# Kernel tuning notes

Hardware: AMD Instinct MI355X
Metric: run time of the kernel (lower is better)

Reference implementation:

```python
import jax, jax.numpy as jnp
import numpy as np

N_NODES = 50000
N_EDGES = 200000
D_IN = 128
D = 256
N_LAYERS = 4
N_REL = 4
NUM_M = 1024
NUM_R = 64
DIM_Y = 2
LAM_VI = 0.1
LAM_REG = 0.1
TEMP = 0.3  # RelaxedBernoulli temperature used by FNP sample_bipartite
EPS = 1e-8


def _glorot(key, shape):
    fan_in = shape[-2] if len(shape) >= 2 else shape[0]
    return (jax.random.normal(key, shape, dtype=jnp.float32) / np.float32(np.sqrt(fan_in)))


def setup_inputs() -> dict:
    key = jax.random.key(0)
    ks = jax.random.split(key, 16)
    x = jax.random.normal(ks[0], (N_NODES, D_IN), jnp.float32)
    edge_index = jax.random.randint(ks[1], (2, N_EDGES), 0, N_NODES)
    edge_type = jax.random.randint(ks[2], (N_EDGES,), 0, N_REL)
    batch = jnp.sort(jax.random.randint(ks[3], (N_NODES,), 0, NUM_M))
    yM = jax.random.randint(ks[4], (NUM_M,), 0, DIM_Y)
    yR = jax.random.randint(ks[5], (NUM_R,), 0, DIM_Y)
    H_R = jax.random.normal(ks[6], (NUM_R, D), jnp.float32)
    node_W = _glorot(ks[7], (D_IN, D)); node_b = jnp.zeros((D,), jnp.float32)
    gcn_Wr = _glorot(ks[8], (N_LAYERS, N_REL, D, D))
    gcn_Wroot = _glorot(ks[9], (N_LAYERS, D, D))
    gcn_b = jnp.zeros((N_LAYERS, D), jnp.float32)
    pg_logscale = jnp.array([0.5 * np.log(D)], jnp.float32)  # log(sqrt(dim_u)) init
    pu_W = _glorot(ks[10], (D, 2 * D)); pu_b = jnp.zeros((2 * D,), jnp.float32)
    qz_W = _glorot(ks[11], (D, 2 * D)); qz_b = jnp.zeros((2 * D,), jnp.float32)
    out_W1 = _glorot(ks[12], (2 * D, 256)); out_b1 = jnp.zeros((256,), jnp.float32)
    out_W2 = _glorot(ks[13], (256, DIM_Y)); out_b2 = jnp.zeros((DIM_Y,), jnp.float32)
    return dict(x=x, edge_index=edge_index, edge_type=edge_type, batch=batch, yM=yM, yR=yR,
                H_R=H_R, node_W=node_W, node_b=node_b, gcn_Wr=gcn_Wr, gcn_Wroot=gcn_Wroot,
                gcn_b=gcn_b, pg_logscale=pg_logscale, pu_W=pu_W, pu_b=pu_b, qz_W=qz_W,
                qz_b=qz_b, out_W1=out_W1, out_b1=out_b1, out_W2=out_W2, out_b2=out_b2)


def _cond_trans(x, edge_index, edge_type, batch, node_W, node_b, gcn_Wr, gcn_Wroot, gcn_b):
    # AtomEncoder replaced by Linear (num_relations==1 branch); then 4 RGCNConv layers
    n = x.shape[0]
    src, dst = edge_index[0], edge_index[1]
    feats = x @ node_W + node_b
    for l in range(N_LAYERS):
        # per-relation transform of all nodes: [N_REL, N, D]
        h_rel = jnp.einsum('nd,rdh->rnh', feats, gcn_Wr[l])
        msg = h_rel[edge_type, src]  # gather per-edge messages [E, D]
        comp = edge_type * n + dst   # (relation, dst) composite segment id
        cnt = jax.ops.segment_sum(jnp.ones((msg.shape[0],), feats.dtype), comp,
                                  num_segments=N_REL * n)
        msg = msg / jnp.clip(cnt[comp], 1.0)[:, None]  # mean aggregation per relation
        agg = jax.ops.segment_sum(msg, dst, num_segments=n)
        feats = agg + feats @ gcn_Wroot[l] + gcn_b[l]
        if l < N_LAYERS - 1:
            feats = jax.nn.relu(feats)
    gsum = jax.ops.segment_sum(feats, batch, num_segments=NUM_M)
    gcnt = jax.ops.segment_sum(jnp.ones((n,), feats.dtype), batch, num_segments=NUM_M)
    return gsum / jnp.clip(gcnt, 1.0)[:, None]  # global_mean_pool


def _normal_logprob(v, mean, logscale):
    return -0.5 * np.float32(np.log(2 * np.pi)) - logscale - 0.5 * ((v - mean) * jnp.exp(-logscale)) ** 2


def _logitexp(logp):
    # logit of exp(logp): logp - log(1 - exp(logp))
    return logp - jnp.log(jnp.clip(-jnp.expm1(logp), 1e-20))


def reference(x, edge_index, edge_type, batch, yM, yR, H_R, node_W, node_b, gcn_Wr,
              gcn_Wroot, gcn_b, pg_logscale, pu_W, pu_b, qz_W, qz_b, out_W1, out_b1,
              out_W2, out_b2):
    H_M = _cond_trans(x, edge_index, edge_type, batch, node_W, node_b, gcn_Wr, gcn_Wroot, gcn_b)
    H_all = jnp.concatenate([H_R, H_M], axis=0)
    key = jax.random.key(42)
    k_u, k_a, k_zm, k_zr = jax.random.split(key, 4)

    # p_u: ReLU -> Linear -> split mean / logscale; reparameterized sample
    pu = jax.nn.relu(H_all) @ pu_W + pu_b
    pu_mean, pu_ls = pu[:, :D], pu[:, D:]
    u = pu_mean + jnp.exp(pu_ls) * jax.random.normal(k_u, pu_mean.shape, pu_mean.dtype)
    u_R, u_M = u[:NUM_R], u[NUM_R:]

    # sample_bipartite(u_M, u_R, pairwise_g): relaxed Bernoulli over pairwise logits
    d2 = jnp.sum((u_M[:, None, :] - u_R[None, :, :]) ** 2, axis=-1)  # [M, R]
    logits_A = _logitexp(-0.5 * d2 / jnp.exp(pg_logscale[0]))
    U = jax.random.uniform(k_a, logits_A.shape, minval=1e-6, maxval=1.0 - 1e-6)
    A = jax.nn.sigmoid((logits_A + jnp.log(U) - jnp.log1p(-U)) / TEMP)
    An = A / (jnp.sum(A, axis=1, keepdims=True) + EPS)  # norm_graph

    # q_z head
    qz = jax.nn.relu(H_all) @ qz_W + qz_b
    qz_mean, qz_ls = qz[:, :D], qz[:, D:]
    z_M = qz_mean[NUM_R:] + jnp.exp(qz_ls[NUM_R:]) * jax.random.normal(k_zm, (NUM_M, D), qz_mean.dtype)
    pz_mean_M = An @ qz_mean[:NUM_R]
    pz_ls_M = An @ qz_ls[:NUM_R]
    log_pqz_M = jnp.sum(_normal_logprob(z_M, pz_mean_M, pz_ls_M)
                        - _normal_logprob(z_M, qz_mean[NUM_R:], qz_ls[NUM_R:]))
    z_R = qz_mean[:NUM_R] + jnp.exp(qz_ls[:NUM_R]) * jax.random.normal(k_zr, (NUM_R, D), qz_mean.dtype)

    # prediction head (use_plus=True -> concat z and u)
    rep_M = jnp.concatenate([z_M, u_M], axis=1)
    logits_M = jax.nn.relu(rep_M @ out_W1 + out_b1) @ out_W2 + out_b2
    log_pyM = jnp.take_along_axis(jax.nn.log_softmax(logits_M, axis=-1), yM[:, None], axis=1)[:, 0]
    prediction_loss = -(jnp.sum(log_pyM) + LAM_VI * log_pqz_M) / np.float32(NUM_M)

    rep_R = jnp.concatenate([z_R, u_R], axis=1)
    logits_R = jax.nn.relu(rep_R @ out_W1 + out_b1) @ out_W2 + out_b2
    rationale_loss = -jnp.mean(jnp.take_along_axis(jax.nn.log_softmax(logits_R, axis=-1), yR[:, None], axis=1)[:, 0])

    # mode 'E' distance regularizer
    pd = jnp.sqrt(jnp.clip(jnp.sum((u_R[:, None, :] - u_M[None, :, :]) ** 2, axis=-1), 1e-12))  # [R, M]
    idx = jnp.arange(NUM_R // 2)[:, None] + (1 - yM)[None, :] * (NUM_R // 2)
    reg = jnp.mean(jnp.take_along_axis(pd, idx, axis=0))

    return prediction_loss + rationale_loss - LAM_REG * reg
```

## Files before the change

### kernel.cpp

```cpp
#include <hip/hip_runtime.h>
#include <stdint.h>

#define N_NODESC 50000
#define N_EDGESC 200000
#define D_INC 128
#define DC 256
#define N_LAYERSC 4
#define N_RELC 4
#define NUM_MC 1024
#define NUM_RC 64
#define NBLK_SCAN ((N_NODESC + 255) / 256)

typedef __attribute__((ext_vector_type(4))) float floatx4;
typedef __attribute__((ext_vector_type(8))) short short8;

__host__ __device__ __forceinline__ uint32_t rotl32(uint32_t x, int r){ return (x<<r)|(x>>(32-r)); }

__host__ __device__ inline void tf2x32(uint32_t k0, uint32_t k1, uint32_t x0, uint32_t x1,
                                       uint32_t* o0, uint32_t* o1){
  uint32_t k2 = k0 ^ k1 ^ 0x1BD11BDAu;
#define TFR(r) { x0 += x1; x1 = rotl32(x1, (r)); x1 ^= x0; }
  x0 += k0; x1 += k1;
  TFR(13) TFR(15) TFR(26) TFR(6)
  x0 += k1; x1 += k2 + 1u;
  TFR(17) TFR(29) TFR(16) TFR(24)
  x0 += k2; x1 += k0 + 2u;
  TFR(13) TFR(15) TFR(26) TFR(6)
  x0 += k0; x1 += k1 + 3u;
  TFR(17) TFR(29) TFR(16) TFR(24)
  x0 += k1; x1 += k2 + 4u;
  TFR(13) TFR(15) TFR(26) TFR(6)
  x0 += k2; x1 += k0 + 5u;
#undef TFR
  *o0 = x0; *o1 = x1;
}

__device__ __forceinline__ float erfinv_f32(float x){
  float w = -log1pf(-x*x);
  float p;
  if (w < 5.0f){
    w -= 2.5f;
    p = 2.81022636e-08f;
    p = fmaf(p, w, 3.43273939e-07f);
    p = fmaf(p, w, -3.5233877e-06f);
    p = fmaf(p, w, -4.39150654e-06f);
    p = fmaf(p, w, 0.00021858087f);
    p = fmaf(p, w, -0.00125372503f);
    p = fmaf(p, w, -0.00417768164f);
    p = fmaf(p, w, 0.246640727f);
    p = fmaf(p, w, 1.50140941f);
  } else {
    w = sqrtf(w) - 3.0f;
    p = -0.000200214257f;
    p = fmaf(p, w, 0.000100950558f);
    p = fmaf(p, w, 0.00134934322f);
    p = fmaf(p, w, -0.00367342844f);
    p = fmaf(p, w, 0.00573950773f);
    p = fmaf(p, w, -0.0076224613f);
    p = fmaf(p, w, 0.00943887047f);
    p = fmaf(p, w, 1.00167406f);
    p = fmaf(p, w, 2.83297682f);
  }
  return p*x;
}

__device__ __forceinline__ float bits_to_unit(uint32_t b){
  return __uint_as_float((b >> 9) | 0x3f800000u) - 1.0f;
}

__device__ __forceinline__ float bits_to_normal(uint32_t b){
  float f = bits_to_unit(b);
  const float lo = -0.99999994f;
  float u = f * (1.0f - lo) + lo;
  u = fmaxf(u, lo);
  return 1.41421356f * erfinv_f32(u);
}

__device__ __forceinline__ float waveReduce(float v){
  #pragma unroll
  for (int m = 1; m < 64; m <<= 1) v += __shfl_xor(v, m, 64);
  return v;
}

__device__ __forceinline__ ushort f2bf(float f){
  uint32_t u = __float_as_uint(f);
  uint32_t r = u + 0x7fffu + ((u>>16)&1u);
  return (ushort)(r>>16);
}
__device__ __forceinline__ float bf2f(ushort h){
  return __uint_as_float(((uint32_t)h)<<16);
}

typedef const __attribute__((address_space(1))) void* gas_t;
typedef __attribute__((address_space(3))) void* las_t;
__device__ __forceinline__ void gld16(const void* g, void* l){
  __builtin_amdgcn_global_load_lds((gas_t)g, (las_t)l, 16, 0, 0);
}

__global__ __launch_bounds__(256) void k_zero4(float4* p, int n4){
  int i = blockIdx.x*256 + threadIdx.x;
  if (i < n4) p[i] = make_float4(0.f,0.f,0.f,0.f);
}

__global__ __launch_bounds__(256) void k_count(const int* __restrict__ ei, const int* __restrict__ et,
                                               float* __restrict__ cnt, int* __restrict__ deg){
  int e = blockIdx.x*256 + threadIdx.x;
  if (e >= N_EDGESC) return;
  int r = et[e], dstv = ei[N_EDGESC + e];
  atomicAdd(&cnt[(size_t)r*N_NODESC + dstv], 1.0f);
  atomicAdd(&deg[dstv], 1);
}

__global__ __launch_bounds__(256) void k_scan1(const int* __restrict__ deg, int* __restrict__ bsum){
  int i = blockIdx.x*256 + threadIdx.x;
  int v = (i < N_NODESC) ? deg[i] : 0;
  #pragma unroll
  for (int m = 1; m < 64; m <<= 1) v += __shfl_xor(v, m, 64);
  __shared__ int ws_[4];
  if ((threadIdx.x & 63) == 0) ws_[threadIdx.x >> 6] = v;
  __syncthreads();
  if (threadIdx.x == 0) bsum[blockIdx.x] = ws_[0]+ws_[1]+ws_[2]+ws_[3];
}

__global__ __launch_bounds__(256) void k_scan2(int* __restrict__ bsum, int* __restrict__ boff){
  __shared__ int s[256];
  int t = threadIdx.x;
  s[t] = (t < NBLK_SCAN) ? bsum[t] : 0;
  __syncthreads();
  if (t == 0){
    int run = 0;
    for (int i = 0; i < NBLK_SCAN; i++){ int v = s[i]; s[i] = run; run += v; }
  }
  __syncthreads();
  if (t < NBLK_SCAN) boff[t] = s[t];
}

__global__ __launch_bounds__(256) void k_scan3(const int* __restrict__ deg, const int* __restrict__ boff,
                                               int* __restrict__ rowptr){
  int i = blockIdx.x*256 + threadIdx.x;
  int lane = threadIdx.x & 63, w = threadIdx.x >> 6;
  int d = (i < N_NODESC) ? deg[i] : 0;
  int v = d;
  #pragma unroll
  for (int off = 1; off < 64; off <<= 1){
    int t = __shfl_up(v, off, 64);
    if (lane >= off) v += t;
  }
  __shared__ int wt[4];
  if (lane == 63) wt[w] = v;
  __syncthreads();
  int wo = 0;
  for (int k = 0; k < w; k++) wo += wt[k];
  int ex = boff[blockIdx.x] + wo + v - d;
  if (i <= N_NODESC) rowptr[i] = ex;
}

__global__ __launch_bounds__(256) void k_fill2(const int* __restrict__ ei, const int* __restrict__ et,
                                               const float* __restrict__ cnt, const int* __restrict__ rowptr,
                                               int* __restrict__ cursor, int* __restrict__ ep,
                                               float* __restrict__ einvc){
  int e = blockIdx.x*256 + threadIdx.x;
  if (e >= N_EDGESC) return;
  int src = ei[e], dstv = ei[N_EDGESC + e], r = et[e];
  int pos = rowptr[dstv] + atomicAdd(&cursor[dstv], 1);
  ep[pos] = src | (r << 16);
  einvc[pos] = 1.0f / fmaxf(cnt[(size_t)r*N_NODESC + dstv], 1.0f);
}

__global__ __launch_bounds__(256) void k_bnd(const int* __restrict__ batch, int* __restrict__ grow){
  int i = blockIdx.x*256 + threadIdx.x;
  if (i >= N_NODESC) return;
  int b = batch[i];
  if (i == 0){ for (int g = 0; g <= b; g++) grow[g] = 0; }
  else {
    int pb = batch[i-1];
    for (int g = pb+1; g <= b; g++) grow[g] = i;
  }
  if (i == N_NODESC-1){ for (int g = b+1; g <= NUM_MC; g++) grow[g] = N_NODESC; }
}

__global__ __launch_bounds__(256) void k_wt(const float* __restrict__ src, ushort* __restrict__ dst,
                                            int K, int N, int total){
  int idx = blockIdx.x*256 + threadIdx.x;
  if (idx >= total) return;
  int k = idx / N, n = idx - k*N;
  dst[(size_t)n*K + k] = f2bf(src[idx]);
}

__global__ __launch_bounds__(256) void k_wcat(const float* __restrict__ Wroot, const float* __restrict__ Wr,
                                              ushort* __restrict__ Wcat){
  int idx = blockIdx.x*256 + threadIdx.x;
  if (idx >= N_LAYERSC*1280*DC) return;
  int l = idx / (1280*DC), rem = idx - l*(1280*DC);
  int n = rem / DC, k = rem - n*DC;
  float v;
  if (n < DC) v = Wroot[((size_t)l*DC + k)*DC + n];
  else {
    int r = (n - DC) >> 8, nn = (n - DC) & 255;
    v = Wr[(((size_t)l*N_RELC + r)*DC + k)*DC + nn];
  }
  Wcat[idx] = f2bf(v);
}

__global__ __launch_bounds__(256) void k_cvt4(const float4* __restrict__ src, ushort4* __restrict__ dst,
                                              int n4){
  int i = blockIdx.x*256 + threadIdx.x;
  if (i >= n4) return;
  float4 v = src[i];
  ushort4 o; o.x=f2bf(v.x); o.y=f2bf(v.y); o.z=f2bf(v.z); o.w=f2bf(v.w);
  dst[i] = o;
}

__global__ __launch_bounds__(256) void k_gather(const ushort* __restrict__ slabs, const float* __restrict__ bias,
                                                ushort* __restrict__ curbOut, int relu,
                                                const int* __restrict__ rowptr, const int* __restrict__ ep,
                                                const float* __restrict__ einvc){
  int dstv = blockIdx.x*4 + (threadIdx.x >> 6);
  if (dstv >= N_NODESC) return;
  int lane = threadIdx.x & 63;
  int beg = rowptr[dstv], end = rowptr[dstv+1];
  const ushort4 w0 = *(const ushort4*)(slabs + (size_t)dstv*DC + lane*4);
  const float4 bv = *(const float4*)(bias + lane*4);
  float ax = bf2f(w0.x) + bv.x, ay = bf2f(w0.y) + bv.y;
  float az = bf2f(w0.z) + bv.z, aw = bf2f(w0.w) + bv.w;
  for (int p = beg; p < end; p++){
    int pk = ep[p];
    float ic = einvc[p];
    int src = pk & 0xffff, r = pk >> 16;
    const ushort4 h = *(const ushort4*)(slabs + ((size_t)(1+r)*N_NODESC + src)*DC + lane*4);
    ax = fmaf(bf2f(h.x), ic, ax);
    ay = fmaf(bf2f(h.y), ic, ay);
    az = fmaf(bf2f(h.z), ic, az);
    aw = fmaf(bf2f(h.w), ic, aw);
  }
  if (relu){ ax=fmaxf(ax,0.f); ay=fmaxf(ay,0.f); az=fmaxf(az,0.f); aw=fmaxf(aw,0.f); }
  ushort4 o; o.x=f2bf(ax); o.y=f2bf(ay); o.z=f2bf(az); o.w=f2bf(aw);
  *(ushort4*)(curbOut + (size_t)dstv*DC + lane*4) = o;
}

__global__ __launch_bounds__(256) void k_pool(const ushort* __restrict__ featsb, const int* __restrict__ grow,
                                              const float* __restrict__ H_R, float* __restrict__ Hrelu){
  int row = blockIdx.x*4 + (threadIdx.x >> 6);
  if (row >= NUM_RC + NUM_MC) return;
  int lane = threadIdx.x & 63;
  float4 v;
  if (row < NUM_RC){
    v = *(const float4*)(H_R + (size_t)row*DC + lane*4);
  } else {
    int g = row - NUM_RC;
    int beg = grow[g], end = grow[g+1];
    float ax=0.f, ay=0.f, az=0.f, aw=0.f;
    for (int i = beg; i < end; i++){
      const ushort4 f = *(const ushort4*)(featsb + (size_t)i*DC + lane*4);
      ax += bf2f(f.x); ay += bf2f(f.y); az += bf2f(f.z); aw += bf2f(f.w);
    }
    float ic = 1.0f / fmaxf((float)(end-beg), 1.0f);
    v.x = ax*ic; v.y = ay*ic; v.z = az*ic; v.w = aw*ic;
  }
  v.x = fmaxf(v.x,0.f); v.y = fmaxf(v.y,0.f); v.z = fmaxf(v.z,0.f); v.w = fmaxf(v.w,0.f);
  *(float4*)(Hrelu + (size_t)row*DC + lane*4) = v;
}

__global__ __launch_bounds__(256) void k_gemm_bf16(
    const ushort* __restrict__ A, int lda,
    const ushort* __restrict__ Bt0, int ldb,
    void* __restrict__ Cout0, int ldc,
    int M, int N, int K,
    const float* __restrict__ bias, int flags,
    size_t strideB, size_t strideC)
{
  __shared__ ushort As[128*32];
  __shared__ ushort Bs[128*32];
  const int tid = threadIdx.x;
  const int wave = tid >> 6, lane = tid & 63;
  const int m0 = blockIdx.y * 128, n0 = blockIdx.x * 128;
  const ushort* Bt = Bt0 + blockIdx.z * strideB;
  const int wm = (wave >> 1) * 64, wn = (wave & 1) * 64;
  const int qa = lane >> 4, lm = lane & 15;

  const int srow = wave*32 + (lane >> 2);
  const int scol = (lane & 3) * 8;

  floatx4 acc[4][4] = {};

  for (int k0 = 0; k0 < K; k0 += 32){
    {
      int r1 = m0 + srow;      if (r1 > M-1) r1 = M-1;
      int r2 = m0 + srow + 16; if (r2 > M-1) r2 = M-1;
      gld16(A + (size_t)r1*lda + k0 + scol, (char*)As + (size_t)srow*64 + (lane&3)*16);
      gld16(A + (size_t)r2*lda + k0 + scol, (char*)As + (size_t)(srow+16)*64 + (lane&3)*16);
      gld16(Bt + (size_t)(n0 + srow)*ldb + k0 + scol,      (char*)Bs + (size_t)srow*64 + (lane&3)*16);
      gld16(Bt + (size_t)(n0 + srow + 16)*ldb + k0 + scol, (char*)Bs + (size_t)(srow+16)*64 + (lane&3)*16);
    }
    __syncthreads();
    short8 af[4], bfv[4];
    #pragma unroll
    for (int mt = 0; mt < 4; mt++)
      af[mt] = *(const short8*)(As + (size_t)(wm + mt*16 + lm)*32 + qa*8);
    #pragma unroll
    for (int nt = 0; nt < 4; nt++)
      bfv[nt] = *(const short8*)(Bs + (size_t)(wn + nt*16 + lm)*32 + qa*8);
    #pragma unroll
    for (int mt = 0; mt < 4; mt++)
      #pragma unroll
      for (int nt = 0; nt < 4; nt++)
        acc[mt][nt] = __builtin_amdgcn_mfma_f32_16x16x32_bf16(af[mt], bfv[nt], acc[mt][nt], 0, 0, 0);
    __syncthreads();
  }

  char* Cout = (char*)Cout0;
  #pragma unroll
  for (int mt = 0; mt < 4; mt++){
    #pragma unroll
    for (int i = 0; i < 4; i++){
      int row = m0 + wm + mt*16 + qa*4 + i;
      if (row >= M) continue;
      #pragma unroll
      for (int nt = 0; nt < 4; nt++){
        int col = n0 + wn + nt*16 + lm;
        float v = acc[mt][nt][i];
        if (flags & 2) v += bias[col];
        if (flags & 8)
          ((ushort*)Cout)[(size_t)(col>>8)*strideC + (size_t)row*256 + (col&255)] = f2bf(v);
        else if (flags & 1)
          ((ushort*)Cout)[blockIdx.z*strideC + (size_t)row*ldc + col] = f2bf(v);
        else
          ((float*)Cout)[blockIdx.z*strideC + (size_t)row*ldc + col] = v;
      }
    }
  }
}

__global__ __launch_bounds__(256) void k_gemm(
    const float* __restrict__ A, int lda,
    const float* __restrict__ B, int ldb,
    float* __restrict__ C, int ldc,
    int M, int N, int K,
    const float* __restrict__ bias, int flags)
{
  __shared__ __align__(16) float Asm[64][36];
  __shared__ __align__(16) float Bsm[32][64];
  const int tid = threadIdx.x;
  const int tx = tid & 15, ty = tid >> 4;
  const int m0 = blockIdx.y * 64, n0 = blockIdx.x * 64;
  const int am = tid >> 2, ak = (tid & 3) * 8;
  const int bk = tid >> 3, bn = (tid & 7) * 8;
  float acc[4][4] = {};
  for (int k0 = 0; k0 < K; k0 += 32){
    float4 a0, a1;
    int arow = m0 + am;
    if (arow < M){
      const float* ap = A + (size_t)arow*lda + (k0 + ak);
      a0 = *(const float4*)ap;
      a1 = *(const float4*)(ap + 4);
    } else {
      a0 = make_float4(0,0,0,0); a1 = a0;
    }
    const float* bp = B + (size_t)(k0 + bk)*ldb + (n0 + bn);
    float4 b0v = *(const float4*)bp;
    float4 b1v = *(const float4*)(bp + 4);
    *(float4*)&Asm[am][ak]   = a0;
    *(float4*)&Asm[am][ak+4] = a1;
    *(float4*)&Bsm[bk][bn]   = b0v;
    *(float4*)&Bsm[bk][bn+4] = b1v;
    __syncthreads();
    #pragma unroll
    for (int kk = 0; kk < 32; ++kk){
      float av[4], bv[4];
      #pragma unroll
      for (int i=0;i<4;i++) av[i] = Asm[ty*4+i][kk];
      #pragma unroll
      for (int j=0;j<4;j++) bv[j] = Bsm[kk][tx*4+j];
      #pragma unroll
      for (int i=0;i<4;i++)
        #pragma unroll
        for (int j=0;j<4;j++)
          acc[i][j] = fmaf(av[i], bv[j], acc[i][j]);
    }
    __syncthreads();
  }
  #pragma unroll
  for (int i=0;i<4;i++){
    int row = m0 + ty*4 + i;
    if (row >= M) continue;
    #pragma unroll
    for (int j=0;j<4;j++){
      int col = n0 + tx*4 + j;
      float v = acc[i][j];
      if (flags & 2) v += bias[col];
      if (flags & 1) v += C[(size_t)row*ldc + col];
      if (flags & 4) v = fmaxf(v, 0.0f);
      C[(size_t)row*ldc + col] = v;
    }
  }
}

__global__ __launch_bounds__(256) void k_sample_u(const float* __restrict__ pu, float* __restrict__ u,
                                                  float* __restrict__ repR, float* __restrict__ repM,
                                                  uint32_t k0, uint32_t k1){
  const int half = (1088*DC)/2;
  int j = blockIdx.x*256 + threadIdx.x;
  if (j >= half) return;
  uint32_t o0, o1;
  tf2x32(k0, k1, (uint32_t)j, (uint32_t)(j + half), &o0, &o1);
  #pragma unroll
  for (int t = 0; t < 2; t++){
    int i = j + t*half;
    uint32_t bits = t ? o1 : o0;
    int row = i >> 8, col = i & 255;
    float val = pu[(size_t)row*512 + col] + expf(pu[(size_t)row*512 + 256 + col]) * bits_to_normal(bits);
    u[i] = val;
    if (row < NUM_RC) repR[(size_t)row*512 + 256 + col] = val;
    else              repM[(size_t)(row - NUM_RC)*512 + 256 + col] = val;
  }
}

__global__ __launch_bounds__(256) void k_sample_zM(const float* __restrict__ qz, float* __restrict__ repM,
                                                   uint32_t k0, uint32_t k1){
  const int half = (NUM_MC*DC)/2;
  int j = blockIdx.x*256 + threadIdx.x;
  if (j >= half) return;
  uint32_t o0, o1;
  tf2x32(k0, k1, (uint32_t)j, (uint32_t)(j + half), &o0, &o1);
  #pragma unroll
  for (int t = 0; t < 2; t++){
    int i = j + t*half;
    uint32_t bits = t ? o1 : o0;
    int m = i >> 8, col = i & 255;
    int row = NUM_RC + m;
    float val = qz[(size_t)row*512 + col] + expf(qz[(size_t)row*512 + 256 + col]) * bits_to_normal(bits);
    repM[(size_t)m*512 + col] = val;
  }
}

__global__ __launch_bounds__(256) void k_sample_zR(const float* __restrict__ qz, float* __restrict__ repR,
                                                   uint32_t k0, uint32_t k1){
  const int half = (NUM_RC*DC)/2;
  int j = blockIdx.x*256 + threadIdx.x;
  if (j >= half) return;
  uint32_t o0, o1;
  tf2x32(k0, k1, (uint32_t)j, (uint32_t)(j + half), &o0, &o1);
  #pragma unroll
  for (int t = 0; t < 2; t++){
    int i = j + t*half;
    uint32_t bits = t ? o1 : o0;
    int r = i >> 8, col = i & 255;
    float val = qz[(size_t)r*512 + col] + expf(qz[(size_t)r*512 + 256 + col]) * bits_to_normal(bits);
    repR[(size_t)r*512 + col] = val;
  }
}

__global__ __launch_bounds__(64) void k_d2(const float* __restrict__ u, float* __restrict__ d2){
  int m = blockIdx.x, r = threadIdx.x;
  const float* um = u + (size_t)(NUM_RC + m)*DC;
  const float* ur = u + (size_t)r*DC;
  float s = 0.f;
  for (int d = 0; d < DC; ++d){ float df = um[d]-ur[d]; s = fmaf(df, df, s); }
  d2[m*NUM_RC + r] = s;
}

__device__ __forceinline__ void A_elem(float* An, const float* d2, int i, uint32_t bits, float inv_s){
  float logp = -0.5f * d2[i] * inv_s;
  float la = logp - logf(fmaxf(-expm1f(logp), 1e-20f));
  float f = bits_to_unit(bits);
  const float mn = 1e-6f, mx = 0.999999f;
  float U = fmaxf(f*(mx-mn) + mn, mn);
  float g = (la + logf(U) - log1pf(-U)) / 0.3f;
  An[i] = 1.0f / (1.0f + expf(-g));
}

__global__ __launch_bounds__(256) void k_A(const float* __restrict__ d2, const float* __restrict__ pg,
                                           float* __restrict__ An, uint32_t k0, uint32_t k1){
  const int HALF = (NUM_MC*NUM_RC)/2;
  int j = blockIdx.x*256 + threadIdx.x;
  if (j >= HALF) return;
  uint32_t o0, o1;
  tf2x32(k0, k1, (uint32_t)j, (uint32_t)(j + HALF), &o0, &o1);
  float inv_s = expf(-pg[0]);
  A_elem(An, d2, j, o0, inv_s);
  A_elem(An, d2, j + HALF, o1, inv_s);
}

__global__ __launch_bounds__(64) void k_rownorm(float* __restrict__ An){
  int m = blockIdx.x, r = threadIdx.x;
  float v = An[m*NUM_RC + r];
  float s = waveReduce(v);
  An[m*NUM_RC + r] = v / (s + 1e-8f);
}

__global__ __launch_bounds__(256) void k_logpqz(const float* __restrict__ repM, const float* __restrict__ pzcat,
                                                const float* __restrict__ qz, float* __restrict__ scal){
  int idx = blockIdx.x*256 + threadIdx.x;
  int m = idx >> 8, d = idx & 255;
  float z  = repM[(size_t)m*512 + d];
  float pm = pzcat[(size_t)m*512 + d];
  float pl = pzcat[(size_t)m*512 + 256 + d];
  const float* qrow = qz + (size_t)(NUM_RC + m)*512;
  float qm = qrow[d], ql = qrow[256 + d];
  float tp = (z - pm) * expf(-pl);
  float tq = (z - qm) * expf(-ql);
  float term = (-pl - 0.5f*tp*tp) - (-ql - 0.5f*tq*tq);
  float s = waveReduce(term);
  if ((threadIdx.x & 63) == 0) atomicAdd(&scal[0], s);
}

__global__ __launch_bounds__(256) void k_out_head(const float* __restrict__ hid, const float* __restrict__ W2,
                                                  const float* __restrict__ b2, const int* __restrict__ y,
                                                  float* __restrict__ target, int M){
  int wave = threadIdx.x >> 6, lane = threadIdx.x & 63;
  int row = blockIdx.x*4 + wave;
  if (row >= M) return;
  const float* h = hid + (size_t)row*256;
  float p0 = 0.f, p1 = 0.f;
  #pragma unroll
  for (int c = 0; c < 4; c++){
    int d = lane*4 + c;
    float hv = h[d];
    p0 = fmaf(hv, W2[d*2+0], p0);
    p1 = fmaf(hv, W2[d*2+1], p1);
  }
  p0 = waveReduce(p0);
  p1 = waveReduce(p1);
  if (lane == 0){
    float l0 = p0 + b2[0], l1 = p1 + b2[1];
    float mx = fmaxf(l0, l1);
    float lse = mx + logf(expf(l0-mx) + expf(l1-mx));
    float lp = ((y[row] == 0) ? l0 : l1) - lse;
    atomicAdd(target, lp);
  }
}

__global__ __launch_bounds__(256) void k_reg(const float* __restrict__ d2, const int* __restrict__ yM,
                                             float* __restrict__ scal){
  int t = blockIdx.x*256 + threadIdx.x;
  float v = 0.f;
  if (t < 32*1024){
    int i = t >> 10, m = t & 1023;
    int col = i + (1 - yM[m]) * 32;
    v = sqrtf(fmaxf(d2[m*NUM_RC + col], 1e-12f));
  }
  float s = waveReduce(v);
  if ((threadIdx.x & 63) == 0) atomicAdd(&scal[3], s);
}

__global__ void k_final(const float* __restrict__ scal, float* __restrict__ out){
  float pred = -(scal[1] + 0.1f*scal[0]) / 1024.0f;
  float rat  = -scal[2] / 64.0f;
  float regm = scal[3] / 32768.0f;
  out[0] = pred + rat - 0.1f*regm;
}

extern "C" void kernel_launch(void* const* d_in, const int* in_sizes, int n_in,
                              void* d_out, int out_size, void* d_ws, size_t ws_size,
                              hipStream_t stream) {
  const float* x         = (const float*)d_in[0];
  const int*   edge_index= (const int*)  d_in[1];
  const int*   edge_type = (const int*)  d_in[2];
  const int*   batch     = (const int*)  d_in[3];
  const int*   yM        = (const int*)  d_in[4];
  const int*   yR        = (const int*)  d_in[5];
  const float* H_R       = (const float*)d_in[6];
  const float* node_W    = (const float*)d_in[7];
  const float* node_b    = (const float*)d_in[8];
  const float* gcn_Wr    = (const float*)d_in[9];
  const float* gcn_Wroot = (const float*)d_in[10];
  const float* gcn_b     = (const float*)d_in[11];
  const float* pg_ls     = (const float*)d_in[12];
  const float* pu_W      = (const float*)d_in[13];
  const float* pu_b      = (const float*)d_in[14];
  const float* qz_W      = (const float*)d_in[15];
  const float* qz_b      = (const float*)d_in[16];
  const float* out_W1    = (const float*)d_in[17];
  const float* out_b1    = (const float*)d_in[18];
  const float* out_W2    = (const float*)d_in[19];
  const float* out_b2    = (const float*)d_in[20];
  float* out = (float*)d_out;

  char* base = (char*)d_ws;
  size_t off = 0;
  auto ALLOC = [&](size_t nbytes)->void*{
    void* p = base + off; off += (nbytes + 255) & ~(size_t)255; return p;
  };
  ushort* slabs   = (ushort*)ALLOC((size_t)5*N_NODESC*DC*2);
  ushort* curb    = (ushort*)ALLOC((size_t)N_NODESC*DC*2);
  ushort* xb      = (ushort*)ALLOC((size_t)N_NODESC*D_INC*2);
  ushort* node_Wt = (ushort*)ALLOC((size_t)DC*D_INC*2);
  ushort* Wcat    = (ushort*)ALLOC((size_t)N_LAYERSC*1280*DC*2);
  float*  zgrp    = (float*) ALLOC((size_t)(N_RELC*N_NODESC + N_NODESC + N_NODESC + 16)*4);
  float*  cnt     = zgrp;
  int*    deg     = (int*)(cnt + (size_t)N_RELC*N_NODESC);
  int*    cursor  = deg + N_NODESC;
  float*  scal    = (float*)(cursor + N_NODESC);
  int*    rowptr  = (int*)   ALLOC((size_t)(N_NODESC+1)*4);
  int*    bsum    = (int*)   ALLOC((size_t)NBLK_SCAN*4);
  int*    boff    = (int*)   ALLOC((size_t)NBLK_SCAN*4);
  int*    ep      = (int*)   ALLOC((size_t)N_EDGESC*4);
  float*  einvc   = (float*) ALLOC((size_t)N_EDGESC*4);
  int*    grow    = (int*)   ALLOC((size_t)(NUM_MC+1)*4);
  float*  Hrelu   = (float*) ALLOC((size_t)1088*DC*4);
  float*  pu      = (float*) ALLOC((size_t)1088*512*4);
  float*  qz      = (float*) ALLOC((size_t)1088*512*4);
  float*  u       = (float*) ALLOC((size_t)1088*DC*4);
  float*  d2      = (float*) ALLOC((size_t)NUM_MC*NUM_RC*4);
  float*  An      = (float*) ALLOC((size_t)NUM_MC*NUM_RC*4);
  float*  pzcat   = (float*) ALLOC((size_t)NUM_MC*512*4);
  float*  repM    = (float*) ALLOC((size_t)NUM_MC*512*4);
  float*  repR    = (float*) ALLOC((size_t)NUM_RC*512*4);
  float*  hidM    = (float*) ALLOC((size_t)NUM_MC*256*4);
  float*  hidR    = (float*) ALLOC((size_t)NUM_RC*256*4);
  (void)ws_size; (void)in_sizes; (void)n_in; (void)out_size;

  uint32_t ya0,ya1,yb0,yb1,yc0,yc1,yd0,yd1;
  tf2x32(0u,42u, 0u,4u, &ya0,&ya1);
  tf2x32(0u,42u, 1u,5u, &yb0,&yb1);
  tf2x32(0u,42u, 2u,6u, &yc0,&yc1);
  tf2x32(0u,42u, 3u,7u, &yd0,&yd1);
  const uint32_t ku0=ya0,  ku1=yb0;
  const uint32_t ka0=yc0,  ka1=yd0;
  const uint32_t kzm0=ya1, kzm1=yb1;
  const uint32_t kzr0=yc1, kzr1=yd1;

  auto GEMM = [&](const float* A, int lda, const float* B, int ldb, float* C, int ldc,
                  int M, int N, int K, const float* bias, int flags){
    k_gemm<<<dim3(N/64, (M+63)/64), dim3(256), 0, stream>>>(A, lda, B, ldb, C, ldc, M, N, K, bias, flags);
  };
  auto BGEMM = [&](const ushort* A, int lda, const ushort* Bt, int ldb, void* C, int ldc,
                   int M, int N, int K, const float* bias, int flags, int gz,
                   size_t strideB, size_t strideC){
    k_gemm_bf16<<<dim3(N/128, (M+127)/128, gz), dim3(256), 0, stream>>>(
        A, lda, Bt, ldb, C, ldc, M, N, K, bias, flags, strideB, strideC);
  };

  {
    int n4 = (N_RELC*N_NODESC + 2*N_NODESC + 16)/4;
    k_zero4<<<dim3((n4+255)/256), dim3(256), 0, stream>>>((float4*)zgrp, n4);
  }
  k_count<<<dim3((N_EDGESC+255)/256), dim3(256), 0, stream>>>(edge_index, edge_type, cnt, deg);
  k_scan1<<<dim3(NBLK_SCAN), dim3(256), 0, stream>>>(deg, bsum);
  k_scan2<<<dim3(1), dim3(256), 0, stream>>>(bsum, boff);
  k_scan3<<<dim3(NBLK_SCAN), dim3(256), 0, stream>>>(deg, boff, rowptr);
  k_fill2<<<dim3((N_EDGESC+255)/256), dim3(256), 0, stream>>>(edge_index, edge_type, cnt, rowptr, cursor, ep, einvc);
  k_bnd  <<<dim3((N_NODESC+255)/256), dim3(256), 0, stream>>>(batch, grow);

  k_wt  <<<dim3((D_INC*DC+255)/256), dim3(256), 0, stream>>>(node_W, node_Wt, D_INC, DC, D_INC*DC);
  k_wcat<<<dim3((N_LAYERSC*1280*DC+255)/256), dim3(256), 0, stream>>>(gcn_Wroot, gcn_Wr, Wcat);
  {
    int n4 = (N_NODESC*D_INC)/4;
    k_cvt4<<<dim3((n4+255)/256), dim3(256), 0, stream>>>((const float4*)x, (ushort4*)xb, n4);
  }

  BGEMM(xb, D_INC, node_Wt, D_INC, curb, DC, N_NODESC, DC, D_INC, node_b, 1|2, 1, 0, 0);

  for (int l = 0; l < N_LAYERSC; l++){
    BGEMM(curb, DC, Wcat + (size_t)l*1280*DC, DC, slabs, DC, N_NODESC, 1280, DC,
          nullptr, 8, 1, 0, (size_t)N_NODESC*DC);
    k_gather<<<dim3((N_NODESC+3)/4), dim3(256), 0, stream>>>(
        slabs, gcn_b + l*DC, curb, (l < N_LAYERSC-1) ? 1 : 0, rowptr, ep, einvc);
  }

  k_pool<<<dim3((NUM_RC+NUM_MC+3)/4), dim3(256), 0, stream>>>(curb, grow, H_R, Hrelu);

  GEMM(Hrelu, DC, pu_W, 512, pu, 512, 1088, 512, DC, pu_b, 2);
  GEMM(Hrelu, DC, qz_W, 512, qz, 512, 1088, 512, DC, qz_b, 2);

  k_sample_u<<<dim3(544), dim3(256), 0, stream>>>(pu, u, repR, repM, ku0, ku1);

  k_d2<<<dim3(NUM_MC), dim3(64), 0, stream>>>(u, d2);
  k_A <<<dim3(128), dim3(256), 0, stream>>>(d2, pg_ls, An, ka0, ka1);
  k_rownorm<<<dim3(NUM_MC), dim3(64), 0, stream>>>(An);

  GEMM(An, NUM_RC, qz, 512, pzcat, 512, NUM_MC, 512, NUM_RC, nullptr, 0);

  k_sample_zM<<<dim3(512), dim3(256), 0, stream>>>(qz, repM, kzm0, kzm1);
  k_logpqz<<<dim3(1024), dim3(256), 0, stream>>>(repM, pzcat, qz, scal);
  k_sample_zR<<<dim3(32), dim3(256), 0, stream>>>(qz, repR, kzr0, kzr1);

  GEMM(repM, 512, out_W1, 256, hidM, 256, NUM_MC, 256, 512, out_b1, 2|4);
  k_out_head<<<dim3(NUM_MC/4), dim3(256), 0, stream>>>(hidM, out_W2, out_b2, yM, scal+1, NUM_MC);

  GEMM(repR, 512, out_W1, 256, hidR, 256, NUM_RC, 256, 512, out_b1, 2|4);
  k_out_head<<<dim3(NUM_RC/4), dim3(256), 0, stream>>>(hidR, out_W2, out_b2, yR, scal+2, NUM_RC);

  k_reg<<<dim3(128), dim3(256), 0, stream>>>(d2, yM, scal);
  k_final<<<dim3(1), dim3(1), 0, stream>>>(scal, out);
}
```

Measured before the change: 877.5 us.

## Aggregate-then-transform RGCN layers with fused K-concat GEMM and merged head kernels

Each RGCN layer now aggregates neighbour features per relation first, writing a 4x256 bf16 aggregate per node, and then runs one GEMM with K=1280 over [cur | agg]. Bias and ReLU are fused into that GEMM's epilogue. This replaces the old order of transforming all nodes into five 256-wide slabs and then gathering them, cutting slab writes and the random gather traffic, at the cost of a larger K and a 100MB aggregate buffer. The weight conversions are merged into one prep kernel and the pu/qz GEMMs are fused into one. The output head is batched into a single bf16 MFMA GEMM plus one head kernel. The GEMM's shared-memory staging layout is also changed.

```diff
diff --git a/kernel.cpp b/kernel.cpp
--- a/kernel.cpp
+++ b/kernel.cpp
@@ -179,63 +179,90 @@
   if (i == N_NODESC-1){ for (int g = b+1; g <= NUM_MC; g++) grow[g] = N_NODESC; }
 }
 
-__global__ __launch_bounds__(256) void k_wt(const float* __restrict__ src, ushort* __restrict__ dst,
-                                            int K, int N, int total){
+#define SEG0 (N_NODESC*D_INC/4)
+#define SEG1 (DC*D_INC)
+#define SEG2 (N_LAYERSC*DC*1280)
+#define SEG3 (DC*1024)
+#define SEG4 (DC*512)
+#define SEG5 1024
+__global__ __launch_bounds__(256) void k_prep(const float* __restrict__ x, ushort* __restrict__ xb,
+                                              const float* __restrict__ node_W, ushort* __restrict__ node_Wt,
+                                              const float* __restrict__ Wroot, const float* __restrict__ Wr,
+                                              ushort* __restrict__ Wcat,
+                                              const float* __restrict__ pu_W, const float* __restrict__ qz_W,
+                                              float* __restrict__ pqW,
+                                              const float* __restrict__ out_W1, ushort* __restrict__ W1t,
+                                              const float* __restrict__ pu_b, const float* __restrict__ qz_b,
+                                              float* __restrict__ pqb){
   int idx = blockIdx.x*256 + threadIdx.x;
-  if (idx >= total) return;
-  int k = idx / N, n = idx - k*N;
-  dst[(size_t)n*K + k] = f2bf(src[idx]);
-}
-
-__global__ __launch_bounds__(256) void k_wcat(const float* __restrict__ Wroot, const float* __restrict__ Wr,
-                                              ushort* __restrict__ Wcat){
-  int idx = blockIdx.x*256 + threadIdx.x;
-  if (idx >= N_LAYERSC*1280*DC) return;
-  int l = idx / (1280*DC), rem = idx - l*(1280*DC);
-  int n = rem / DC, k = rem - n*DC;
-  float v;
-  if (n < DC) v = Wroot[((size_t)l*DC + k)*DC + n];
-  else {
-    int r = (n - DC) >> 8, nn = (n - DC) & 255;
-    v = Wr[(((size_t)l*N_RELC + r)*DC + k)*DC + nn];
-  }
-  Wcat[idx] = f2bf(v);
-}
-
-__global__ __launch_bounds__(256) void k_cvt4(const float4* __restrict__ src, ushort4* __restrict__ dst,
-                                              int n4){
-  int i = blockIdx.x*256 + threadIdx.x;
-  if (i >= n4) return;
-  float4 v = src[i];
-  ushort4 o; o.x=f2bf(v.x); o.y=f2bf(v.y); o.z=f2bf(v.z); o.w=f2bf(v.w);
-  dst[i] = o;
-}
-
-__global__ __launch_bounds__(256) void k_gather(const ushort* __restrict__ slabs, const float* __restrict__ bias,
-                                                ushort* __restrict__ curbOut, int relu,
-                                                const int* __restrict__ rowptr, const int* __restrict__ ep,
-                                                const float* __restrict__ einvc){
+  if (idx < SEG0){
+    float4 v = ((const float4*)x)[idx];
+    ushort4 o; o.x=f2bf(v.x); o.y=f2bf(v.y); o.z=f2bf(v.z); o.w=f2bf(v.w);
+    ((ushort4*)xb)[idx] = o;
+    return;
+  }
+  idx -= SEG0;
+  if (idx < SEG1){
+    int n = idx >> 7, k = idx & 127;
+    node_Wt[idx] = f2bf(node_W[(size_t)k*DC + n]);
+    return;
+  }
+  idx -= SEG1;
+  if (idx < SEG2){
+    int l = idx / (DC*1280), rem = idx - l*(DC*1280);
+    int n = rem / 1280, k = rem - n*1280;
+    float v;
+    if (k < DC) v = Wroot[((size_t)l*DC + k)*DC + n];
+    else {
+      int kk = k - DC, r = kk >> 8, kr = kk & 255;
+      v = Wr[(((size_t)l*N_RELC + r)*DC + kr)*DC + n];
+    }
+    Wcat[idx] = f2bf(v);
+    return;
+  }
+  idx -= SEG2;
+  if (idx < SEG3){
+    int k = idx >> 10, n = idx & 1023;
+    pqW[idx] = (n < 512) ? pu_W[(size_t)k*512 + n] : qz_W[(size_t)k*512 + (n-512)];
+    return;
+  }
+  idx -= SEG3;
+  if (idx < SEG4){
+    int n = idx >> 9, k = idx & 511;
+    W1t[idx] = f2bf(out_W1[(size_t)k*DC + n]);
+    return;
+  }
+  idx -= SEG4;
+  if (idx < SEG5){
+    pqb[idx] = (idx < 512) ? pu_b[idx] : qz_b[idx-512];
+  }
+}
+
+__global__ __launch_bounds__(256) void k_agg(const ushort* __restrict__ curb, ushort* __restrict__ agg,
+                                             const int* __restrict__ rowptr, const int* __restrict__ ep,
+                                             const float* __restrict__ einvc){
   int dstv = blockIdx.x*4 + (threadIdx.x >> 6);
   if (dstv >= N_NODESC) return;
   int lane = threadIdx.x & 63;
   int beg = rowptr[dstv], end = rowptr[dstv+1];
-  const ushort4 w0 = *(const ushort4*)(slabs + (size_t)dstv*DC + lane*4);
-  const float4 bv = *(const float4*)(bias + lane*4);
-  float ax = bf2f(w0.x) + bv.x, ay = bf2f(w0.y) + bv.y;
-  float az = bf2f(w0.z) + bv.z, aw = bf2f(w0.w) + bv.w;
+  float4 s0 = {0,0,0,0}, s1 = {0,0,0,0}, s2 = {0,0,0,0}, s3 = {0,0,0,0};
   for (int p = beg; p < end; p++){
     int pk = ep[p];
     float ic = einvc[p];
     int src = pk & 0xffff, r = pk >> 16;
-    const ushort4 h = *(const ushort4*)(slabs + ((size_t)(1+r)*N_NODESC + src)*DC + lane*4);
-    ax = fmaf(bf2f(h.x), ic, ax);
-    ay = fmaf(bf2f(h.y), ic, ay);
-    az = fmaf(bf2f(h.z), ic, az);
-    aw = fmaf(bf2f(h.w), ic, aw);
-  }
-  if (relu){ ax=fmaxf(ax,0.f); ay=fmaxf(ay,0.f); az=fmaxf(az,0.f); aw=fmaxf(aw,0.f); }
-  ushort4 o; o.x=f2bf(ax); o.y=f2bf(ay); o.z=f2bf(az); o.w=f2bf(aw);
-  *(ushort4*)(curbOut + (size_t)dstv*DC + lane*4) = o;
+    const ushort4 h = *(const ushort4*)(curb + (size_t)src*DC + lane*4);
+    float hx = bf2f(h.x)*ic, hy = bf2f(h.y)*ic, hz = bf2f(h.z)*ic, hw = bf2f(h.w)*ic;
+    if (r == 0){ s0.x+=hx; s0.y+=hy; s0.z+=hz; s0.w+=hw; }
+    else if (r == 1){ s1.x+=hx; s1.y+=hy; s1.z+=hz; s1.w+=hw; }
+    else if (r == 2){ s2.x+=hx; s2.y+=hy; s2.z+=hz; s2.w+=hw; }
+    else { s3.x+=hx; s3.y+=hy; s3.z+=hz; s3.w+=hw; }
+  }
+  ushort* ab = agg + (size_t)dstv*1024 + lane*4;
+  ushort4 o;
+  o.x=f2bf(s0.x); o.y=f2bf(s0.y); o.z=f2bf(s0.z); o.w=f2bf(s0.w); *(ushort4*)(ab       ) = o;
+  o.x=f2bf(s1.x); o.y=f2bf(s1.y); o.z=f2bf(s1.z); o.w=f2bf(s1.w); *(ushort4*)(ab + 256 ) = o;
+  o.x=f2bf(s2.x); o.y=f2bf(s2.y); o.z=f2bf(s2.z); o.w=f2bf(s2.w); *(ushort4*)(ab + 512 ) = o;
+  o.x=f2bf(s3.x); o.y=f2bf(s3.y); o.z=f2bf(s3.z); o.w=f2bf(s3.w); *(ushort4*)(ab + 768 ) = o;
 }
 
 __global__ __launch_bounds__(256) void k_pool(const ushort* __restrict__ featsb, const int* __restrict__ grow,
@@ -262,44 +289,44 @@
 }
 
 __global__ __launch_bounds__(256) void k_gemm_bf16(
-    const ushort* __restrict__ A, int lda,
-    const ushort* __restrict__ Bt0, int ldb,
+    const ushort* __restrict__ A1, int lda1,
+    const ushort* __restrict__ A2, int lda2, int Ksplit,
+    const ushort* __restrict__ Bt, int ldb,
     void* __restrict__ Cout0, int ldc,
     int M, int N, int K,
-    const float* __restrict__ bias, int flags,
-    size_t strideB, size_t strideC)
+    const float* __restrict__ bias, int flags)
 {
   __shared__ ushort As[128*32];
   __shared__ ushort Bs[128*32];
   const int tid = threadIdx.x;
   const int wave = tid >> 6, lane = tid & 63;
   const int m0 = blockIdx.y * 128, n0 = blockIdx.x * 128;
-  const ushort* Bt = Bt0 + blockIdx.z * strideB;
   const int wm = (wave >> 1) * 64, wn = (wave & 1) * 64;
   const int qa = lane >> 4, lm = lane & 15;
 
-  const int srow = wave*32 + (lane >> 2);
-  const int scol = (lane & 3) * 8;
+  int ar1 = m0 + lane;        if (ar1 > M-1) ar1 = M-1;
+  int ar2 = m0 + 64 + lane;   if (ar2 > M-1) ar2 = M-1;
+  const int bn1 = n0 + lane, bn2 = n0 + 64 + lane;
+  const int kw = wave * 8;
 
   floatx4 acc[4][4] = {};
 
   for (int k0 = 0; k0 < K; k0 += 32){
-    {
-      int r1 = m0 + srow;      if (r1 > M-1) r1 = M-1;
-      int r2 = m0 + srow + 16; if (r2 > M-1) r2 = M-1;
-      gld16(A + (size_t)r1*lda + k0 + scol, (char*)As + (size_t)srow*64 + (lane&3)*16);
-      gld16(A + (size_t)r2*lda + k0 + scol, (char*)As + (size_t)(srow+16)*64 + (lane&3)*16);
-      gld16(Bt + (size_t)(n0 + srow)*ldb + k0 + scol,      (char*)Bs + (size_t)srow*64 + (lane&3)*16);
-      gld16(Bt + (size_t)(n0 + srow + 16)*ldb + k0 + scol, (char*)Bs + (size_t)(srow+16)*64 + (lane&3)*16);
-    }
+    const ushort* a_base; int a_ld, a_col;
+    if (k0 < Ksplit){ a_base = A1; a_ld = lda1; a_col = k0 + kw; }
+    else            { a_base = A2; a_ld = lda2; a_col = k0 - Ksplit + kw; }
+    gld16(a_base + (size_t)ar1*a_ld + a_col, (char*)As + ((size_t)wave*128      + lane)*16);
+    gld16(a_base + (size_t)ar2*a_ld + a_col, (char*)As + ((size_t)wave*128 + 64 + lane)*16);
+    gld16(Bt + (size_t)bn1*ldb + k0 + kw,    (char*)Bs + ((size_t)wave*128      + lane)*16);
+    gld16(Bt + (size_t)bn2*ldb + k0 + kw,    (char*)Bs + ((size_t)wave*128 + 64 + lane)*16);
     __syncthreads();
     short8 af[4], bfv[4];
     #pragma unroll
     for (int mt = 0; mt < 4; mt++)
-      af[mt] = *(const short8*)(As + (size_t)(wm + mt*16 + lm)*32 + qa*8);
+      af[mt] = *(const short8*)(As + ((size_t)qa*128 + wm + mt*16 + lm)*8);
     #pragma unroll
     for (int nt = 0; nt < 4; nt++)
-      bfv[nt] = *(const short8*)(Bs + (size_t)(wn + nt*16 + lm)*32 + qa*8);
+      bfv[nt] = *(const short8*)(Bs + ((size_t)qa*128 + wn + nt*16 + lm)*8);
     #pragma unroll
     for (int mt = 0; mt < 4; mt++)
       #pragma unroll
@@ -308,7 +335,6 @@
     __syncthreads();
   }
 
-  char* Cout = (char*)Cout0;
   #pragma unroll
   for (int mt = 0; mt < 4; mt++){
     #pragma unroll
@@ -320,12 +346,11 @@
         int col = n0 + wn + nt*16 + lm;
         float v = acc[mt][nt][i];
         if (flags & 2) v += bias[col];
-        if (flags & 8)
-          ((ushort*)Cout)[(size_t)(col>>8)*strideC + (size_t)row*256 + (col&255)] = f2bf(v);
-        else if (flags & 1)
-          ((ushort*)Cout)[blockIdx.z*strideC + (size_t)row*ldc + col] = f2bf(v);
+        if (flags & 4) v = fmaxf(v, 0.0f);
+        if (flags & 1)
+          ((ushort*)Cout0)[(size_t)row*ldc + col] = f2bf(v);
         else
-          ((float*)Cout)[blockIdx.z*strideC + (size_t)row*ldc + col] = v;
+          ((float*)Cout0)[(size_t)row*ldc + col] = v;
       }
     }
   }
@@ -388,15 +413,14 @@
       int col = n0 + tx*4 + j;
       float v = acc[i][j];
       if (flags & 2) v += bias[col];
-      if (flags & 1) v += C[(size_t)row*ldc + col];
       if (flags & 4) v = fmaxf(v, 0.0f);
       C[(size_t)row*ldc + col] = v;
     }
   }
 }
 
-__global__ __launch_bounds__(256) void k_sample_u(const float* __restrict__ pu, float* __restrict__ u,
-                                                  float* __restrict__ repR, float* __restrict__ repM,
+__global__ __launch_bounds__(256) void k_sample_u(const float* __restrict__ pq, float* __restrict__ u,
+                                                  ushort* __restrict__ repb,
                                                   uint32_t k0, uint32_t k1){
   const int half = (1088*DC)/2;
   int j = blockIdx.x*256 + threadIdx.x;
@@ -408,14 +432,15 @@
     int i = j + t*half;
     uint32_t bits = t ? o1 : o0;
     int row = i >> 8, col = i & 255;
-    float val = pu[(size_t)row*512 + col] + expf(pu[(size_t)row*512 + 256 + col]) * bits_to_normal(bits);
+    const float* pr = pq + (size_t)row*1024;
+    float val = pr[col] + expf(pr[256 + col]) * bits_to_normal(bits);
     u[i] = val;
-    if (row < NUM_RC) repR[(size_t)row*512 + 256 + col] = val;
-    else              repM[(size_t)(row - NUM_RC)*512 + 256 + col] = val;
-  }
-}
-
-__global__ __launch_bounds__(256) void k_sample_zM(const float* __restrict__ qz, float* __restrict__ repM,
+    repb[(size_t)row*512 + 256 + col] = f2bf(val);
+  }
+}
+
+__global__ __launch_bounds__(256) void k_sample_zM(const float* __restrict__ pq, float* __restrict__ zM,
+                                                   ushort* __restrict__ repb,
                                                    uint32_t k0, uint32_t k1){
   const int half = (NUM_MC*DC)/2;
   int j = blockIdx.x*256 + threadIdx.x;
@@ -427,13 +452,14 @@
     int i = j + t*half;
     uint32_t bits = t ? o1 : o0;
     int m = i >> 8, col = i & 255;
-    int row = NUM_RC + m;
-    float val = qz[(size_t)row*512 + col] + expf(qz[(size_t)row*512 + 256 + col]) * bits_to_normal(bits);
-    repM[(size_t)m*512 + col] = val;
-  }
-}
-
-__global__ __launch_bounds__(256) void k_sample_zR(const float* __restrict__ qz, float* __restrict__ repR,
+    const float* pr = pq + (size_t)(NUM_RC + m)*1024;
+    float val = pr[512 + col] + expf(pr[768 + col]) * bits_to_normal(bits);
+    zM[i] = val;
+    repb[(size_t)(NUM_RC + m)*512 + col] = f2bf(val);
+  }
+}
+
+__global__ __launch_bounds__(256) void k_sample_zR(const float* __restrict__ pq, ushort* __restrict__ repb,
                                                    uint32_t k0, uint32_t k1){
   const int half = (NUM_RC*DC)/2;
   int j = blockIdx.x*256 + threadIdx.x;
@@ -445,17 +471,23 @@
     int i = j + t*half;
     uint32_t bits = t ? o1 : o0;
     int r = i >> 8, col = i & 255;
-    float val = qz[(size_t)r*512 + col] + expf(qz[(size_t)r*512 + 256 + col]) * bits_to_normal(bits);
-    repR[(size_t)r*512 + col] = val;
+    const float* pr = pq + (size_t)r*1024;
+    float val = pr[512 + col] + expf(pr[768 + col]) * bits_to_normal(bits);
+    repb[(size_t)r*512 + col] = f2bf(val);
   }
 }
 
 __global__ __launch_bounds__(64) void k_d2(const float* __restrict__ u, float* __restrict__ d2){
   int m = blockIdx.x, r = threadIdx.x;
-  const float* um = u + (size_t)(NUM_RC + m)*DC;
-  const float* ur = u + (size_t)r*DC;
+  const float4* um = (const float4*)(u + (size_t)(NUM_RC + m)*DC);
+  const float4* ur = (const float4*)(u + (size_t)r*DC);
   float s = 0.f;
-  for (int d = 0; d < DC; ++d){ float df = um[d]-ur[d]; s = fmaf(df, df, s); }
+  #pragma unroll 4
+  for (int d = 0; d < DC/4; ++d){
+    float4 a = um[d], b = ur[d];
+    float dx = a.x-b.x, dy = a.y-b.y, dz = a.z-b.z, dw = a.w-b.w;
+    s = fmaf(dx,dx, fmaf(dy,dy, fmaf(dz,dz, fmaf(dw,dw, s))));
+  }
   d2[m*NUM_RC + r] = s;
 }
 
@@ -488,15 +520,15 @@
   An[m*NUM_RC + r] = v / (s + 1e-8f);
 }
 
-__global__ __launch_bounds__(256) void k_logpqz(const float* __restrict__ repM, const float* __restrict__ pzcat,
-                                                const float* __restrict__ qz, float* __restrict__ scal){
+__global__ __launch_bounds__(256) void k_logpqz(const float* __restrict__ zM, const float* __restrict__ pzcat,
+                                                const float* __restrict__ pq, float* __restrict__ scal){
   int idx = blockIdx.x*256 + threadIdx.x;
   int m = idx >> 8, d = idx & 255;
-  float z  = repM[(size_t)m*512 + d];
+  float z  = zM[idx];
   float pm = pzcat[(size_t)m*512 + d];
   float pl = pzcat[(size_t)m*512 + 256 + d];
-  const float* qrow = qz + (size_t)(NUM_RC + m)*512;
-  float qm = qrow[d], ql = qrow[256 + d];
+  const float* qrow = pq + (size_t)(NUM_RC + m)*1024;
+  float qm = qrow[512 + d], ql = qrow[768 + d];
   float tp = (z - pm) * expf(-pl);
   float tq = (z - qm) * expf(-ql);
   float term = (-pl - 0.5f*tp*tp) - (-ql - 0.5f*tq*tq);
@@ -505,11 +537,11 @@
 }
 
 __global__ __launch_bounds__(256) void k_out_head(const float* __restrict__ hid, const float* __restrict__ W2,
-                                                  const float* __restrict__ b2, const int* __restrict__ y,
-                                                  float* __restrict__ target, int M){
+                                                  const float* __restrict__ b2, const int* __restrict__ yM,
+                                                  const int* __restrict__ yR, float* __restrict__ scal){
   int wave = threadIdx.x >> 6, lane = threadIdx.x & 63;
   int row = blockIdx.x*4 + wave;
-  if (row >= M) return;
+  if (row >= NUM_RC + NUM_MC) return;
   const float* h = hid + (size_t)row*256;
   float p0 = 0.f, p1 = 0.f;
   #pragma unroll
@@ -525,8 +557,9 @@
     float l0 = p0 + b2[0], l1 = p1 + b2[1];
     float mx = fmaxf(l0, l1);
     float lse = mx + logf(expf(l0-mx) + expf(l1-mx));
-    float lp = ((y[row] == 0) ? l0 : l1) - lse;
-    atomicAdd(target, lp);
+    int y = (row < NUM_RC) ? yR[row] : yM[row - NUM_RC];
+    float lp = ((y == 0) ? l0 : l1) - lse;
+    atomicAdd((row < NUM_RC) ? &scal[2] : &scal[1], lp);
   }
 }
 
@@ -581,11 +614,15 @@
   auto ALLOC = [&](size_t nbytes)->void*{
     void* p = base + off; off += (nbytes + 255) & ~(size_t)255; return p;
   };
-  ushort* slabs   = (ushort*)ALLOC((size_t)5*N_NODESC*DC*2);
-  ushort* curb    = (ushort*)ALLOC((size_t)N_NODESC*DC*2);
+  ushort* curb_a  = (ushort*)ALLOC((size_t)N_NODESC*DC*2);
+  ushort* curb_b  = (ushort*)ALLOC((size_t)N_NODESC*DC*2);
+  ushort* agg     = (ushort*)ALLOC((size_t)N_NODESC*1024*2);
   ushort* xb      = (ushort*)ALLOC((size_t)N_NODESC*D_INC*2);
-  ushort* node_Wt = (ushort*)ALLOC((size_t)DC*D_INC*2);
-  ushort* Wcat    = (ushort*)ALLOC((size_t)N_LAYERSC*1280*DC*2);
+  ushort* node_Wt = (ushort*)ALLOC((size_t)SEG1*2);
+  ushort* Wcat    = (ushort*)ALLOC((size_t)SEG2*2);
+  float*  pqW     = (float*) ALLOC((size_t)SEG3*4);
+  ushort* W1t     = (ushort*)ALLOC((size_t)SEG4*2);
+  float*  pqb     = (float*) ALLOC((size_t)SEG5*4);
   float*  zgrp    = (float*) ALLOC((size_t)(N_RELC*N_NODESC + N_NODESC + N_NODESC + 16)*4);
   float*  cnt     = zgrp;
   int*    deg     = (int*)(cnt + (size_t)N_RELC*N_NODESC);
@@ -598,16 +635,14 @@
   float*  einvc   = (float*) ALLOC((size_t)N_EDGESC*4);
   int*    grow    = (int*)   ALLOC((size_t)(NUM_MC+1)*4);
   float*  Hrelu   = (float*) ALLOC((size_t)1088*DC*4);
-  float*  pu      = (float*) ALLOC((size_t)1088*512*4);
-  float*  qz      = (float*) ALLOC((size_t)1088*512*4);
+  float*  pq      = (float*) ALLOC((size_t)1088*1024*4);
   float*  u       = (float*) ALLOC((size_t)1088*DC*4);
+  ushort* repb    = (ushort*)ALLOC((size_t)1088*512*2);
+  float*  zM      = (float*) ALLOC((size_t)NUM_MC*DC*4);
   float*  d2      = (float*) ALLOC((size_t)NUM_MC*NUM_RC*4);
   float*  An      = (float*) ALLOC((size_t)NUM_MC*NUM_RC*4);
   float*  pzcat   = (float*) ALLOC((size_t)NUM_MC*512*4);
-  float*  repM    = (float*) ALLOC((size_t)NUM_MC*512*4);
-  float*  repR    = (float*) ALLOC((size_t)NUM_RC*512*4);
-  float*  hidM    = (float*) ALLOC((size_t)NUM_MC*256*4);
-  float*  hidR    = (float*) ALLOC((size_t)NUM_RC*256*4);
+  float*  hid     = (float*) ALLOC((size_t)1088*256*4);
   (void)ws_size; (void)in_sizes; (void)n_in; (void)out_size;
 
   uint32_t ya0,ya1,yb0,yb1,yc0,yc1,yd0,yd1;
@@ -624,11 +659,11 @@
                   int M, int N, int K, const float* bias, int flags){
     k_gemm<<<dim3(N/64, (M+63)/64), dim3(256), 0, stream>>>(A, lda, B, ldb, C, ldc, M, N, K, bias, flags);
   };
-  auto BGEMM = [&](const ushort* A, int lda, const ushort* Bt, int ldb, void* C, int ldc,
-                   int M, int N, int K, const float* bias, int flags, int gz,
-                   size_t strideB, size_t strideC){
-    k_gemm_bf16<<<dim3(N/128, (M+127)/128, gz), dim3(256), 0, stream>>>(
-        A, lda, Bt, ldb, C, ldc, M, N, K, bias, flags, strideB, strideC);
+  auto BGEMM = [&](const ushort* A1, int lda1, const ushort* A2, int lda2, int Ksplit,
+                   const ushort* Bt, int ldb, void* C, int ldc,
+                   int M, int N, int K, const float* bias, int flags){
+    k_gemm_bf16<<<dim3(N/128, (M+127)/128), dim3(256), 0, stream>>>(
+        A1, lda1, A2, lda2, Ksplit, Bt, ldb, C, ldc, M, N, K, bias, flags);
   };
 
   {
@@ -641,45 +676,41 @@
   k_scan3<<<dim3(NBLK_SCAN), dim3(256), 0, stream>>>(deg, boff, rowptr);
   k_fill2<<<dim3((N_EDGESC+255)/256), dim3(256), 0, stream>>>(edge_index, edge_type, cnt, rowptr, cursor, ep, einvc);
   k_bnd  <<<dim3((N_NODESC+255)/256), dim3(256), 0, stream>>>(batch, grow);
-
-  k_wt  <<<dim3((D_INC*DC+255)/256), dim3(256), 0, stream>>>(node_W, node_Wt, D_INC, DC, D_INC*DC);
-  k_wcat<<<dim3((N_LAYERSC*1280*DC+255)/256), dim3(256), 0, stream>>>(gcn_Wroot, gcn_Wr, Wcat);
   {
-    int n4 = (N_NODESC*D_INC)/4;
-    k_cvt4<<<dim3((n4+255)/256), dim3(256), 0, stream>>>((const float4*)x, (ushort4*)xb, n4);
-  }
-
-  BGEMM(xb, D_INC, node_Wt, D_INC, curb, DC, N_NODESC, DC, D_INC, node_b, 1|2, 1, 0, 0);
-
+    int total = SEG0+SEG1+SEG2+SEG3+SEG4+SEG5;
+    k_prep<<<dim3((total+255)/256), dim3(256), 0, stream>>>(
+        x, xb, node_W, node_Wt, gcn_Wroot, gcn_Wr, Wcat, pu_W, qz_W, pqW, out_W1, W1t, pu_b, qz_b, pqb);
+  }
+
+  BGEMM(xb, D_INC, xb, D_INC, D_INC, node_Wt, D_INC, curb_a, DC, N_NODESC, DC, D_INC, node_b, 1|2);
+
+  ushort* cur = curb_a; ushort* nxt = curb_b;
   for (int l = 0; l < N_LAYERSC; l++){
-    BGEMM(curb, DC, Wcat + (size_t)l*1280*DC, DC, slabs, DC, N_NODESC, 1280, DC,
-          nullptr, 8, 1, 0, (size_t)N_NODESC*DC);
-    k_gather<<<dim3((N_NODESC+3)/4), dim3(256), 0, stream>>>(
-        slabs, gcn_b + l*DC, curb, (l < N_LAYERSC-1) ? 1 : 0, rowptr, ep, einvc);
-  }
-
-  k_pool<<<dim3((NUM_RC+NUM_MC+3)/4), dim3(256), 0, stream>>>(curb, grow, H_R, Hrelu);
-
-  GEMM(Hrelu, DC, pu_W, 512, pu, 512, 1088, 512, DC, pu_b, 2);
-  GEMM(Hrelu, DC, qz_W, 512, qz, 512, 1088, 512, DC, qz_b, 2);
-
-  k_sample_u<<<dim3(544), dim3(256), 0, stream>>>(pu, u, repR, repM, ku0, ku1);
+    k_agg<<<dim3((N_NODESC+3)/4), dim3(256), 0, stream>>>(cur, agg, rowptr, ep, einvc);
+    int fl = 1 | 2 | ((l < N_LAYERSC-1) ? 4 : 0);
+    BGEMM(cur, DC, agg, 1024, DC, Wcat + (size_t)l*DC*1280, 1280, nxt, DC,
+          N_NODESC, DC, 1280, gcn_b + l*DC, fl);
+    ushort* t = nxt; nxt = cur; cur = t;
+  }
+
+  k_pool<<<dim3((NUM_RC+NUM_MC+3)/4), dim3(256), 0, stream>>>(cur, grow, H_R, Hrelu);
+
+  GEMM(Hrelu, DC, pqW, 1024, pq, 1024, 1088, 1024, DC, pqb, 2);
+
+  k_sample_u<<<dim3(544), dim3(256), 0, stream>>>(pq, u, repb, ku0, ku1);
 
   k_d2<<<dim3(NUM_MC), dim3(64), 0, stream>>>(u, d2);
   k_A <<<dim3(128), dim3(256), 0, stream>>>(d2, pg_ls, An, ka0, ka1);
   k_rownorm<<<dim3(NUM_MC), dim3(64), 0, stream>>>(An);
 
-  GEMM(An, NUM_RC, qz, 512, pzcat, 512, NUM_MC, 512, NUM_RC, nullptr, 0);
-
-  k_sample_zM<<<dim3(512), dim3(256), 0, stream>>>(qz, repM, kzm0, kzm1);
-  k_logpqz<<<dim3(1024), dim3(256), 0, stream>>>(repM, pzcat, qz, scal);
-  k_sample_zR<<<dim3(32), dim3(256), 0, stream>>>(qz, repR, kzr0, kzr1);
-
-  GEMM(repM, 512, out_W1, 256, hidM, 256, NUM_MC, 256, 512, out_b1, 2|4);
-  k_out_head<<<dim3(NUM_MC/4), dim3(256), 0, stream>>>(hidM, out_W2, out_b2, yM, scal+1, NUM_MC);
-
-  GEMM(repR, 512, out_W1, 256, hidR, 256, NUM_RC, 256, 512, out_b1, 2|4);
-  k_out_head<<<dim3(NUM_RC/4), dim3(256), 0, stream>>>(hidR, out_W2, out_b2, yR, scal+2, NUM_RC);
+  GEMM(An, NUM_RC, pq + 512, 1024, pzcat, 512, NUM_MC, 512, NUM_RC, nullptr, 0);
+
+  k_sample_zM<<<dim3(512), dim3(256), 0, stream>>>(pq, zM, repb, kzm0, kzm1);
+  k_logpqz<<<dim3(1024), dim3(256), 0, stream>>>(zM, pzcat, pq, scal);
+  k_sample_zR<<<dim3(32), dim3(256), 0, stream>>>(pq, repb, kzr0, kzr1);
+
+  BGEMM(repb, 512, repb, 512, 512, W1t, 512, hid, 256, NUM_RC+NUM_MC, 256, 512, out_b1, 2|4);
+  k_out_head<<<dim3((NUM_RC+NUM_MC)/4), dim3(256), 0, stream>>>(hid, out_W2, out_b2, yM, yR, scal);
 
   k_reg<<<dim3(128), dim3(256), 0, stream>>>(d2, yM, scal);
   k_final<<<dim3(1), dim3(1), 0, stream>>>(scal, out);
```

Result: slower. 1.050 ms (+19.6%).
